# Optimization experiments

Hardware: AMD Instinct MI355X
Metric: run time of the kernel (lower is better)

The kernel has to match this reference:

```python
import jax, jax.numpy as jnp
import numpy as np

# config (stands in for global `args` in the original repo)
N = 8192            # args.tRNA + args.disease
NNZ = 262144        # number of edges in adj
N_SEEDS = 256
MASK_DEPTH = 2      # args.maskDepth
KEEP_RATE = 0.9     # args.keepRate


def setup_inputs() -> dict:
    rng = np.random.default_rng(0)
    # duplicate-free edge list (coalesced sparse tensor)
    h = rng.choice(N * N, size=NNZ, replace=False)
    adj_rows = jnp.asarray(h // N, dtype=jnp.int32)
    adj_cols = jnp.asarray(h % N, dtype=jnp.int32)
    key = jax.random.key(0)
    k1, k2, k3 = jax.random.split(key, 3)
    adj_values = jax.random.uniform(k1, (NNZ,), dtype=jnp.float32)
    seeds = jax.random.randint(k2, (N_SEEDS,), 0, N, dtype=jnp.int32)
    complemental = jax.random.uniform(k3, (N, N), dtype=jnp.float32)
    return {"adj_rows": adj_rows, "adj_cols": adj_cols, "adj_values": adj_values,
            "seeds": seeds, "complemental": complemental}


def _forward(adj_rows, adj_cols, adj_values, seeds, complemental):
    rows, cols = adj_rows, adj_cols
    # --- BFS edge masking (sequential per-seed removal == union removal) ---
    keep = jnp.ones((NNZ,), bool)
    seed_mask = jnp.zeros((N,), bool).at[seeds].set(True)
    mask_nodes = seed_mask
    for i in range(MASK_DEPTH):
        incident = keep & (seed_mask[rows] | seed_mask[cols])
        keep = keep & ~incident
        if i != MASK_DEPTH - 1:
            inc_i = incident.astype(jnp.int32)
            nxt = (jnp.zeros((N,), jnp.int32).at[rows].add(inc_i)
                   .at[cols].add(inc_i)) > 0
            seed_mask = nxt
            mask_nodes = mask_nodes | nxt
    # --- random node sampling augments the mask set ---
    key = jax.random.key(42)
    k1, k2, k3 = jax.random.split(key, 3)
    samp_num = int(N * KEEP_RATE)
    samped = jax.random.randint(k1, (samp_num,), 0, N)
    mask_nodes = mask_nodes.at[samped].set(True)
    # --- encoder adj: kept edges, values gathered from complemental, D^-1/2 A D^-1/2 ---
    keep_i = keep.astype(jnp.int32)
    enc_cov = (jnp.zeros((N, N), jnp.int32).at[rows, cols].add(keep_i)) > 0
    enc_dense = jnp.where(enc_cov, complemental, 0.0)
    deg = enc_dense.sum(axis=1)
    norm = (deg + 1e-12) ** -0.5
    enc = enc_dense * norm[:, None] * norm[None, :]
    # --- decoder adj: random mask-node pairs (symmetric) + self loops + kept edges ---
    mask_idx = jnp.nonzero(mask_nodes, size=N, fill_value=0)[0]
    tem_num = mask_nodes.sum()
    u1 = jax.random.uniform(k2, (NNZ,))
    u2 = jax.random.uniform(k3, (NNZ,))
    tem_rows = mask_idx[jnp.floor(u1 * tem_num).astype(jnp.int32)]
    tem_cols = mask_idx[jnp.floor(u2 * tem_num).astype(jnp.int32)]
    ar = jnp.arange(N, dtype=jnp.int32)
    new_rows = jnp.concatenate([tem_rows, tem_cols, ar, rows])
    new_cols = jnp.concatenate([tem_cols, tem_rows, ar, cols])
    valid = jnp.concatenate([jnp.ones((2 * NNZ + N,), jnp.int32), keep_i])
    # hash-dedup in the original == coverage set; values depend only on (r,c)
    dec_cov = (jnp.zeros((N, N), jnp.int32).at[new_rows, new_cols].add(valid)) > 0
    dec = jnp.where(dec_cov, complemental, 0.0)
    return enc, dec


def reference(adj_rows, adj_cols, adj_values, seeds, complemental):
    return _forward(adj_rows, adj_cols, adj_values, seeds, complemental)
```

## Files before the change

kernel.cpp:

```cpp
#include <hip/hip_runtime.h>
#include <stdint.h>
#include <math.h>

static __device__ __forceinline__ uint32_t rotl32(uint32_t x, int r) {
    return (x << r) | (x >> (32 - r));
}

static __device__ __forceinline__ void tf2x32(uint32_t k0, uint32_t k1,
                                              uint32_t& x0, uint32_t& x1) {
    uint32_t ks2 = k0 ^ k1 ^ 0x1BD11BDAu;
    x0 += k0; x1 += k1;
#define TFR(r) { x0 += x1; x1 = rotl32(x1, r); x1 ^= x0; }
    TFR(13) TFR(15) TFR(26) TFR(6)
    x0 += k1;  x1 += ks2 + 1u;
    TFR(17) TFR(29) TFR(16) TFR(24)
    x0 += ks2; x1 += k0 + 2u;
    TFR(13) TFR(15) TFR(26) TFR(6)
    x0 += k0;  x1 += k1 + 3u;
    TFR(17) TFR(29) TFR(16) TFR(24)
    x0 += k1;  x1 += ks2 + 4u;
    TFR(13) TFR(15) TFR(26) TFR(6)
    x0 += ks2; x1 += k0 + 5u;
#undef TFR
}

struct SubKeys { uint32_t k1a, k1b, k2a, k2b, k3a, k3b; };

static __device__ __forceinline__ SubKeys derive_keys() {
    uint32_t a0 = 0, b0 = 3; tf2x32(0u, 42u, a0, b0);
    uint32_t a1 = 1, b1 = 4; tf2x32(0u, 42u, a1, b1);
    uint32_t a2 = 2, b2 = 5; tf2x32(0u, 42u, a2, b2);
    SubKeys s; s.k1a = a0; s.k1b = a1; s.k2a = a2; s.k2b = b0; s.k3a = b1; s.k3b = b2;
    return s;
}

static __device__ __forceinline__ float bits_to_unit_float(uint32_t b) {
    return __uint_as_float((b >> 9) | 0x3f800000u) - 1.0f;
}

__global__ void k_seed(const int* __restrict__ seeds, int n_seeds,
                       unsigned char* __restrict__ seedm) {
    int i = blockIdx.x * blockDim.x + threadIdx.x;
    if (i < n_seeds) seedm[seeds[i]] = 1;
}

__global__ void __launch_bounds__(256)
k_fill_edge1(const int* __restrict__ rows, const int* __restrict__ cols, int nnz,
             const unsigned char* __restrict__ seedm,
             unsigned char* __restrict__ keep, unsigned char* __restrict__ nxt,
             float* __restrict__ out, size_t out_elems,
             float* __restrict__ deg, int n) {
    const int tid = blockIdx.x * blockDim.x + threadIdx.x;
    const int nt  = gridDim.x * blockDim.x;
    for (int e = tid; e < nnz; e += nt) {
        int r = rows[e], c = cols[e];
        bool inc = (seedm[r] | seedm[c]) != 0;
        keep[e] = inc ? 0 : 1;
        if (inc) { nxt[r] = 1; nxt[c] = 1; }
    }
    const float4 z = make_float4(0.f, 0.f, 0.f, 0.f);
    float4* p = (float4*)out;
    const size_t t4 = out_elems / 4;
    for (size_t i = tid; i < t4; i += (size_t)nt) p[i] = z;
    for (int i = tid; i < n; i += nt) deg[i] = 0.0f;
}

__global__ void __launch_bounds__(256)
k_edge2_deg_dec(const int* __restrict__ rows, const int* __restrict__ cols, int nnz,
                const unsigned char* __restrict__ seedm,
                const unsigned char* __restrict__ nxt,
                unsigned char* __restrict__ keep, unsigned char* __restrict__ mask,
                const float* __restrict__ comp, float* __restrict__ deg,
                float* __restrict__ dec, int n) {
    const int tid = blockIdx.x * blockDim.x + threadIdx.x;
    const int nt  = gridDim.x * blockDim.x;
    for (int e = tid; e < nnz; e += nt) {
        int r = rows[e], c = cols[e];
        unsigned char k = keep[e];
        if (k && ((nxt[r] | nxt[c]) != 0)) { k = 0; keep[e] = 0; }
        if (k) {
            size_t o = (size_t)r * n + c;
            float v = comp[o];
            atomicAdd(&deg[r], v);
            dec[o] = v;
        }
    }
    for (int i = tid; i < n; i += nt) mask[i] = (unsigned char)(seedm[i] | nxt[i]);
}

__global__ void __launch_bounds__(256)
k_samp_norm_diag(int samp_half, int n, unsigned char* __restrict__ mask,
                 const float* __restrict__ deg, float* __restrict__ nrm,
                 const float* __restrict__ comp, float* __restrict__ dec) {
    const int tid = blockIdx.x * blockDim.x + threadIdx.x;
    if (tid < samp_half) {
        SubKeys sk = derive_keys();
        uint32_t x0 = (uint32_t)tid, x1 = (uint32_t)(tid + samp_half);
        tf2x32(sk.k1a, sk.k1b, x0, x1);
        mask[x0 & (uint32_t)(n - 1)] = 1;
        mask[x1 & (uint32_t)(n - 1)] = 1;
    }
    if (tid < n) {
        nrm[tid] = 1.0f / sqrtf(deg[tid] + 1e-12f);
        size_t o = (size_t)tid * n + tid;
        dec[o] = comp[o];
    }
}

__global__ void __launch_bounds__(1024)
k_scan(int n, const unsigned char* __restrict__ mask,
       int* __restrict__ mask_idx, int* __restrict__ tem_num) {
    __shared__ int ssum[1024];
    int t = threadIdx.x;
    int per = n / 1024;
    int base = t * per;
    int loc[8];
    int s = 0;
    for (int j = 0; j < per; ++j) { loc[j] = mask[base + j]; s += loc[j]; }
    ssum[t] = s;
    __syncthreads();
    for (int off = 1; off < 1024; off <<= 1) {
        int v = (t >= off) ? ssum[t - off] : 0;
        __syncthreads();
        ssum[t] += v;
        __syncthreads();
    }
    int excl = ssum[t] - s;
    for (int j = 0; j < per; ++j)
        if (loc[j]) mask_idx[excl++] = base + j;
    if (t == 1023) *tem_num = ssum[1023];
}

__global__ void __launch_bounds__(256)
k_enc_dectem(const int* __restrict__ rows, const int* __restrict__ cols, int nnz,
             const unsigned char* __restrict__ keep,
             const float* __restrict__ comp, const float* __restrict__ nrm,
             float* __restrict__ enc, float* __restrict__ dec,
             const int* __restrict__ mask_idx, const int* __restrict__ tem_num,
             int n) {
    const int tid = blockIdx.x * blockDim.x + threadIdx.x;
    const int nt  = gridDim.x * blockDim.x;
    for (int e = tid; e < nnz; e += nt) {
        if (keep[e]) {
            int r = rows[e], c = cols[e];
            size_t o = (size_t)r * n + c;
            enc[o] = comp[o] * nrm[r] * nrm[c];
        }
    }
    const int ehalf = nnz / 2;
    const float tf = (float)(*tem_num);
    SubKeys sk = derive_keys();
    for (int e = tid; e < ehalf; e += nt) {
        uint32_t u1a = (uint32_t)e, u1b = (uint32_t)(e + ehalf);
        tf2x32(sk.k2a, sk.k2b, u1a, u1b);
        uint32_t u2a = (uint32_t)e, u2b = (uint32_t)(e + ehalf);
        tf2x32(sk.k3a, sk.k3b, u2a, u2b);
#pragma unroll
        for (int j = 0; j < 2; ++j) {
            uint32_t b1 = j ? u1b : u1a;
            uint32_t b2 = j ? u2b : u2a;
            float uu1 = bits_to_unit_float(b1);
            float uu2 = bits_to_unit_float(b2);
            int i1 = (int)(uu1 * tf);
            int i2 = (int)(uu2 * tf);
            int r = mask_idx[i1];
            int c = mask_idx[i2];
            size_t o1 = (size_t)r * n + c;
            size_t o2 = (size_t)c * n + r;
            dec[o1] = comp[o1];
            dec[o2] = comp[o2];
        }
    }
}

extern "C" void kernel_launch(void* const* d_in, const int* in_sizes, int n_in,
                              void* d_out, int out_size, void* d_ws, size_t ws_size,
                              hipStream_t stream) {
    const int*   rows  = (const int*)d_in[0];
    const int*   cols  = (const int*)d_in[1];
    const int*   seeds = (const int*)d_in[3];
    const float* comp  = (const float*)d_in[4];

    const int nnz     = in_sizes[0];
    const int n_seeds = in_sizes[3];
    const int n       = (int)(sqrt((double)in_sizes[4]) + 0.5);

    float* enc = (float*)d_out;
    float* dec = enc + (size_t)n * n;

    char* ws = (char*)d_ws;
    unsigned char* seedm = (unsigned char*)ws;
    unsigned char* nxt   = seedm + n;
    unsigned char* mask  = nxt + n;
    unsigned char* keep  = mask + n;
    char* ws2 = ws + 3 * (size_t)n + (size_t)nnz;
    float* deg      = (float*)ws2;
    float* nrm      = (float*)(ws2 + 4 * (size_t)n);
    int*   mask_idx = (int*)  (ws2 + 8 * (size_t)n);
    int*   tem_num  = (int*)  (ws2 + 12 * (size_t)n);

    hipMemsetAsync(ws, 0, 2 * (size_t)n, stream);

    const int B = 256;
    k_seed<<<(n_seeds + B - 1) / B, B, 0, stream>>>(seeds, n_seeds, seedm);

    k_fill_edge1<<<2048, B, 0, stream>>>(rows, cols, nnz, seedm, keep, nxt,
                                         enc, (size_t)2 * n * n, deg, n);

    k_edge2_deg_dec<<<(nnz + B - 1) / B, B, 0, stream>>>(rows, cols, nnz, seedm, nxt,
                                                         keep, mask, comp, deg, dec, n);

    int samp_num  = (int)((double)n * 0.9);
    int samp_half = samp_num / 2;
    k_samp_norm_diag<<<(n + B - 1) / B, B, 0, stream>>>(samp_half, n, mask,
                                                        deg, nrm, comp, dec);

    k_scan<<<1, 1024, 0, stream>>>(n, mask, mask_idx, tem_num);

    k_enc_dectem<<<(nnz + B - 1) / B, B, 0, stream>>>(rows, cols, nnz, keep, comp, nrm,
                                                      enc, dec, mask_idx, tem_num, n);
}
```

Measured before the change: 731.6 us.

## Fold sampling into seed kernel, merge norm into scan, precompute RNG keys on host

```diff
diff --git a/kernel.cpp b/kernel.cpp
--- a/kernel.cpp
+++ b/kernel.cpp
@@ -2,11 +2,11 @@
 #include <stdint.h>
 #include <math.h>
 
-static __device__ __forceinline__ uint32_t rotl32(uint32_t x, int r) {
+__host__ __device__ static inline uint32_t rotl32(uint32_t x, int r) {
     return (x << r) | (x >> (32 - r));
 }
 
-static __device__ __forceinline__ void tf2x32(uint32_t k0, uint32_t k1,
+__host__ __device__ static inline void tf2x32(uint32_t k0, uint32_t k1,
                                               uint32_t& x0, uint32_t& x1) {
     uint32_t ks2 = k0 ^ k1 ^ 0x1BD11BDAu;
     x0 += k0; x1 += k1;
@@ -26,7 +26,7 @@
 
 struct SubKeys { uint32_t k1a, k1b, k2a, k2b, k3a, k3b; };
 
-static __device__ __forceinline__ SubKeys derive_keys() {
+static inline SubKeys derive_keys_host() {
     uint32_t a0 = 0, b0 = 3; tf2x32(0u, 42u, a0, b0);
     uint32_t a1 = 1, b1 = 4; tf2x32(0u, 42u, a1, b1);
     uint32_t a2 = 2, b2 = 5; tf2x32(0u, 42u, a2, b2);
@@ -34,14 +34,22 @@
     return s;
 }
 
-static __device__ __forceinline__ float bits_to_unit_float(uint32_t b) {
+__device__ static inline float bits_to_unit_float(uint32_t b) {
     return __uint_as_float((b >> 9) | 0x3f800000u) - 1.0f;
 }
 
-__global__ void k_seed(const int* __restrict__ seeds, int n_seeds,
-                       unsigned char* __restrict__ seedm) {
-    int i = blockIdx.x * blockDim.x + threadIdx.x;
-    if (i < n_seeds) seedm[seeds[i]] = 1;
+__global__ void __launch_bounds__(256)
+k_seed_samp(const int* __restrict__ seeds, int n_seeds,
+            unsigned char* __restrict__ seedm,
+            int samp_half, int n, unsigned char* __restrict__ sampm, SubKeys sk) {
+    int t = blockIdx.x * blockDim.x + threadIdx.x;
+    if (t < n_seeds) seedm[seeds[t]] = 1;
+    if (t < samp_half) {
+        uint32_t x0 = (uint32_t)t, x1 = (uint32_t)(t + samp_half);
+        tf2x32(sk.k1a, sk.k1b, x0, x1);
+        sampm[x0 & (uint32_t)(n - 1)] = 1;
+        sampm[x1 & (uint32_t)(n - 1)] = 1;
+    }
 }
 
 __global__ void __launch_bounds__(256)
@@ -69,6 +77,7 @@
 k_edge2_deg_dec(const int* __restrict__ rows, const int* __restrict__ cols, int nnz,
                 const unsigned char* __restrict__ seedm,
                 const unsigned char* __restrict__ nxt,
+                const unsigned char* __restrict__ sampm,
                 unsigned char* __restrict__ keep, unsigned char* __restrict__ mask,
                 const float* __restrict__ comp, float* __restrict__ deg,
                 float* __restrict__ dec, int n) {
@@ -85,38 +94,24 @@
             dec[o] = v;
         }
     }
-    for (int i = tid; i < n; i += nt) mask[i] = (unsigned char)(seedm[i] | nxt[i]);
-}
-
-__global__ void __launch_bounds__(256)
-k_samp_norm_diag(int samp_half, int n, unsigned char* __restrict__ mask,
-                 const float* __restrict__ deg, float* __restrict__ nrm,
-                 const float* __restrict__ comp, float* __restrict__ dec) {
-    const int tid = blockIdx.x * blockDim.x + threadIdx.x;
-    if (tid < samp_half) {
-        SubKeys sk = derive_keys();
-        uint32_t x0 = (uint32_t)tid, x1 = (uint32_t)(tid + samp_half);
-        tf2x32(sk.k1a, sk.k1b, x0, x1);
-        mask[x0 & (uint32_t)(n - 1)] = 1;
-        mask[x1 & (uint32_t)(n - 1)] = 1;
-    }
-    if (tid < n) {
-        nrm[tid] = 1.0f / sqrtf(deg[tid] + 1e-12f);
-        size_t o = (size_t)tid * n + tid;
-        dec[o] = comp[o];
-    }
+    for (int i = tid; i < n; i += nt)
+        mask[i] = (unsigned char)(seedm[i] | nxt[i] | sampm[i]);
 }
 
 __global__ void __launch_bounds__(1024)
-k_scan(int n, const unsigned char* __restrict__ mask,
-       int* __restrict__ mask_idx, int* __restrict__ tem_num) {
+k_norm_scan(int n, const float* __restrict__ deg, float* __restrict__ nrm,
+            const unsigned char* __restrict__ mask,
+            int* __restrict__ mask_idx, int* __restrict__ tem_num) {
     __shared__ int ssum[1024];
     int t = threadIdx.x;
     int per = n / 1024;
     int base = t * per;
     int loc[8];
     int s = 0;
-    for (int j = 0; j < per; ++j) { loc[j] = mask[base + j]; s += loc[j]; }
+    for (int j = 0; j < per; ++j) {
+        loc[j] = mask[base + j]; s += loc[j];
+        nrm[base + j] = 1.0f / sqrtf(deg[base + j] + 1e-12f);
+    }
     ssum[t] = s;
     __syncthreads();
     for (int off = 1; off < 1024; off <<= 1) {
@@ -137,7 +132,7 @@
              const float* __restrict__ comp, const float* __restrict__ nrm,
              float* __restrict__ enc, float* __restrict__ dec,
              const int* __restrict__ mask_idx, const int* __restrict__ tem_num,
-             int n) {
+             int n, SubKeys sk) {
     const int tid = blockIdx.x * blockDim.x + threadIdx.x;
     const int nt  = gridDim.x * blockDim.x;
     for (int e = tid; e < nnz; e += nt) {
@@ -147,29 +142,30 @@
             enc[o] = comp[o] * nrm[r] * nrm[c];
         }
     }
+    for (int i = tid; i < n; i += nt) {
+        size_t o = (size_t)i * n + i;
+        dec[o] = comp[o];
+    }
     const int ehalf = nnz / 2;
     const float tf = (float)(*tem_num);
-    SubKeys sk = derive_keys();
-    for (int e = tid; e < ehalf; e += nt) {
-        uint32_t u1a = (uint32_t)e, u1b = (uint32_t)(e + ehalf);
+    for (int p = tid; p < nnz; p += nt) {
+        uint32_t c0, c1;
+        if (p < ehalf) { c0 = (uint32_t)p; c1 = (uint32_t)(p + ehalf); }
+        else           { c0 = (uint32_t)(p - ehalf); c1 = (uint32_t)p; }
+        uint32_t u1a = c0, u1b = c1;
         tf2x32(sk.k2a, sk.k2b, u1a, u1b);
-        uint32_t u2a = (uint32_t)e, u2b = (uint32_t)(e + ehalf);
+        uint32_t u2a = c0, u2b = c1;
         tf2x32(sk.k3a, sk.k3b, u2a, u2b);
-#pragma unroll
-        for (int j = 0; j < 2; ++j) {
-            uint32_t b1 = j ? u1b : u1a;
-            uint32_t b2 = j ? u2b : u2a;
-            float uu1 = bits_to_unit_float(b1);
-            float uu2 = bits_to_unit_float(b2);
-            int i1 = (int)(uu1 * tf);
-            int i2 = (int)(uu2 * tf);
-            int r = mask_idx[i1];
-            int c = mask_idx[i2];
-            size_t o1 = (size_t)r * n + c;
-            size_t o2 = (size_t)c * n + r;
-            dec[o1] = comp[o1];
-            dec[o2] = comp[o2];
-        }
+        uint32_t b1 = (p < ehalf) ? u1a : u1b;
+        uint32_t b2 = (p < ehalf) ? u2a : u2b;
+        int i1 = (int)(bits_to_unit_float(b1) * tf);
+        int i2 = (int)(bits_to_unit_float(b2) * tf);
+        int r = mask_idx[i1];
+        int c = mask_idx[i2];
+        size_t o1 = (size_t)r * n + c;
+        size_t o2 = (size_t)c * n + r;
+        dec[o1] = comp[o1];
+        dec[o2] = comp[o2];
     }
 }
 
@@ -191,32 +187,36 @@
     char* ws = (char*)d_ws;
     unsigned char* seedm = (unsigned char*)ws;
     unsigned char* nxt   = seedm + n;
-    unsigned char* mask  = nxt + n;
+    unsigned char* sampm = nxt + n;
+    unsigned char* mask  = sampm + n;
     unsigned char* keep  = mask + n;
-    char* ws2 = ws + 3 * (size_t)n + (size_t)nnz;
+    char* ws2 = ws + 4 * (size_t)n + (size_t)nnz;
     float* deg      = (float*)ws2;
     float* nrm      = (float*)(ws2 + 4 * (size_t)n);
     int*   mask_idx = (int*)  (ws2 + 8 * (size_t)n);
     int*   tem_num  = (int*)  (ws2 + 12 * (size_t)n);
 
-    hipMemsetAsync(ws, 0, 2 * (size_t)n, stream);
+    SubKeys sk = derive_keys_host();
+    int samp_num  = (int)((double)n * 0.9);
+    int samp_half = samp_num / 2;
+
+    hipMemsetAsync(ws, 0, 3 * (size_t)n, stream);
 
     const int B = 256;
-    k_seed<<<(n_seeds + B - 1) / B, B, 0, stream>>>(seeds, n_seeds, seedm);
+    int g0 = (samp_half > n_seeds ? samp_half : n_seeds);
+    k_seed_samp<<<(g0 + B - 1) / B, B, 0, stream>>>(seeds, n_seeds, seedm,
+                                                    samp_half, n, sampm, sk);
 
     k_fill_edge1<<<2048, B, 0, stream>>>(rows, cols, nnz, seedm, keep, nxt,
                                          enc, (size_t)2 * n * n, deg, n);
 
     k_edge2_deg_dec<<<(nnz + B - 1) / B, B, 0, stream>>>(rows, cols, nnz, seedm, nxt,
-                                                         keep, mask, comp, deg, dec, n);
-
-    int samp_num  = (int)((double)n * 0.9);
-    int samp_half = samp_num / 2;
-    k_samp_norm_diag<<<(n + B - 1) / B, B, 0, stream>>>(samp_half, n, mask,
-                                                        deg, nrm, comp, dec);
-
-    k_scan<<<1, 1024, 0, stream>>>(n, mask, mask_idx, tem_num);
+                                                         sampm, keep, mask, comp,
+                                                         deg, dec, n);
+
+    k_norm_scan<<<1, 1024, 0, stream>>>(n, deg, nrm, mask, mask_idx, tem_num);
 
     k_enc_dectem<<<(nnz + B - 1) / B, B, 0, stream>>>(rows, cols, nnz, keep, comp, nrm,
-                                                      enc, dec, mask_idx, tem_num, n);
-}
+                                                      enc, dec, mask_idx, tem_num,
+                                                      n, sk);
+}
```

After: 739.0 us. No clear change (+1.0%).
